# Performance work log

Hardware: AMD Instinct MI355X
Metric: run time of the kernel (lower is better)

Reference implementation:

```python
import jax, jax.numpy as jnp
import numpy as np

N_NODES = 4096
IN_FEATURES = 256
N_HEADS = 8
N_HIDDEN = 32  # out_features // n_heads = 256 // 8
NEG_SLOPE = 0.2
MASK_FILL = -1e9


def setup_inputs() -> dict:
    key = jax.random.key(0)
    k_h, k_adj, k_w, k_a = jax.random.split(key, 4)
    h = jax.random.normal(k_h, (N_NODES, IN_FEATURES), dtype=jnp.float32)
    adj_mat = jax.random.randint(k_adj, (N_NODES, N_NODES, 1), 0, 2, dtype=jnp.int32)
    # linear: Linear(in_features, n_hidden*n_heads, bias=False) -> W: [in, H*F]
    W = jax.random.normal(k_w, (IN_FEATURES, N_HEADS * N_HIDDEN), dtype=jnp.float32) / np.sqrt(IN_FEATURES)
    # attn: Linear(2*n_hidden, 1, bias=False) -> a: [2*F]
    a = jax.random.normal(k_a, (2 * N_HIDDEN,), dtype=jnp.float32) / np.sqrt(2 * N_HIDDEN)
    return {"h": h, "adj_mat": adj_mat, "W": W, "a": a}


def reference(h, adj_mat, W, a):
    n = h.shape[0]
    # g: [n, H, F]
    g = (h @ W).reshape(n, N_HEADS, N_HIDDEN)
    # attn(concat(g_i, g_j)) == g_i . a[:F] + g_j . a[F:]  (decomposed, same math,
    # avoids materializing the O(N^2 * H * 2F) concat tensor of the torch code)
    a_src, a_dst = a[:N_HIDDEN], a[N_HIDDEN:]
    s_src = jnp.einsum('nhf,f->nh', g, a_src)  # [n, H]
    s_dst = jnp.einsum('nhf,f->nh', g, a_dst)  # [n, H]
    e = jax.nn.leaky_relu(s_src[:, None, :] + s_dst[None, :, :], negative_slope=NEG_SLOPE)  # [n, n, H]
    e = jnp.where(adj_mat == 0, MASK_FILL, e)  # adj_mat [n, n, 1] broadcasts over heads
    att = jax.nn.softmax(e, axis=1)  # softmax over source nodes j (dropout in eval mode = identity)
    out = jnp.einsum('ijh,jhf->ihf', att, g)  # [n, H, F]
    return out.reshape(n, N_HEADS * N_HIDDEN)  # is_concat=True
```

## Files before the change

### kernel.cpp

```cpp
#include <hip/hip_runtime.h>

#define NN 4096
#define FIN 256
#define CC 256
#define NH 8
#define NW32 (NN / 32)

typedef __attribute__((ext_vector_type(8))) short short8;
typedef __attribute__((ext_vector_type(4))) float f32x4;
typedef __attribute__((ext_vector_type(4))) unsigned int u32x4;

__device__ __forceinline__ unsigned cvtpk_bf16(float lo, float hi) {
  unsigned r;
  asm("v_cvt_pk_bf16_f32 %0, %1, %2" : "=v"(r) : "v"(lo), "v"(hi));
  return r;
}

__device__ __forceinline__ unsigned short bf16rn(float x) {
  unsigned int u = __builtin_bit_cast(unsigned int, x);
  u += 0x7fffu + ((u >> 16) & 1u);
  return (unsigned short)(u >> 16);
}

__device__ __forceinline__ void gl_lds16(const void* g, void* l) {
  __builtin_amdgcn_global_load_lds(
      (const __attribute__((address_space(1))) void*)g,
      (__attribute__((address_space(3))) void*)l, 16, 0, 0);
}

#define GROWS 8
__global__ __launch_bounds__(256) void k_gemm(
    const float* __restrict__ h, const float* __restrict__ W,
    const float* __restrict__ a, const int* __restrict__ adj,
    unsigned int* __restrict__ adjb, unsigned short* __restrict__ gTs,
    float4* __restrict__ spack, float* __restrict__ dtc) {
  __shared__ float hs[GROWS][FIN];
  const int t = threadIdx.x;

  {
    const int rbase = blockIdx.x * 8;
#pragma unroll
    for (int k = 0; k < 4; ++k) {
      const int idx = k * 256 + t;
      const int r = idx >> 7, wd = idx & 127;
      const int* src = adj + (size_t)(rbase + r) * NN + wd * 32;
      unsigned int bits = 0;
#pragma unroll
      for (int s = 0; s < 8; ++s) {
        const int4 v = *(const int4*)&src[s * 4];
        bits |= (v.x ? 1u : 0u) << (s * 4 + 0);
        bits |= (v.y ? 1u : 0u) << (s * 4 + 1);
        bits |= (v.z ? 1u : 0u) << (s * 4 + 2);
        bits |= (v.w ? 1u : 0u) << (s * 4 + 3);
      }
      adjb[(size_t)(rbase + r) * NW32 + wd] = bits;
    }
  }

  const int r0 = blockIdx.x * GROWS;
#pragma unroll
  for (int idx = t; idx < GROWS * FIN / 4; idx += 256) {
    const int r = idx >> 6, c4 = idx & 63;
    *(float4*)&hs[r][c4 * 4] =
        *(const float4*)&h[(size_t)(r0 + r) * FIN + c4 * 4];
  }
  __syncthreads();
  const int c = t;
  float acc[GROWS];
#pragma unroll
  for (int r = 0; r < GROWS; ++r) acc[r] = 0.f;
  for (int k = 0; k < FIN; k += 4) {
    const float w0 = W[(size_t)(k + 0) * CC + c];
    const float w1 = W[(size_t)(k + 1) * CC + c];
    const float w2 = W[(size_t)(k + 2) * CC + c];
    const float w3 = W[(size_t)(k + 3) * CC + c];
#pragma unroll
    for (int r = 0; r < GROWS; ++r) {
      const float4 hv = *(const float4*)&hs[r][k];
      acc[r] += hv.x * w0 + hv.y * w1 + hv.z * w2 + hv.w * w3;
    }
  }
  const int f = c & 31, hh = c >> 5;
  const float aS = a[f], aD = a[32 + f];
  unsigned short gu[GROWS];
#pragma unroll
  for (int r = 0; r < GROWS; ++r) {
    float ps = acc[r] * aS, pd = acc[r] * aD;
#pragma unroll
    for (int m = 1; m < 32; m <<= 1) {
      ps += __shfl_xor(ps, m, 64);
      pd += __shfl_xor(pd, m, 64);
    }
    if (f == 0) {
      const int n = r0 + r;
      spack[(size_t)hh * NN + n] =
          make_float4(ps, __expf(ps), __expf(0.2f * ps), 0.f);
      float* dc = dtc + (size_t)(n >> 5) * 768 + hh * 32 + (n & 31);
      dc[0] = -pd;
      dc[256] = __expf(pd);
      dc[512] = __expf(0.2f * pd);
    }
    gu[r] = bf16rn(acc[r]);
  }
  uint4 gv;
  gv.x = (unsigned)gu[0] | ((unsigned)gu[1] << 16);
  gv.y = (unsigned)gu[2] | ((unsigned)gu[3] << 16);
  gv.z = (unsigned)gu[4] | ((unsigned)gu[5] << 16);
  gv.w = (unsigned)gu[6] | ((unsigned)gu[7] << 16);
  const int jc = r0 >> 5, qq = (r0 >> 3) & 3;
  const int p = qq ^ ((c >> 1) & 3);
  *(uint4*)(gTs + ((size_t)jc * 1024 + c * 4 + p) * 8) = gv;
}

struct Buf {
  unsigned short gt[8192];
  float dt[3][NH][32];
};

__global__ __launch_bounds__(256, 2) void k_attn(
    const unsigned int* __restrict__ adjb, const unsigned short* __restrict__ gTs,
    const float4* __restrict__ spack, const float* __restrict__ dtc,
    float* __restrict__ acc_ws, float* __restrict__ l_ws,
    float* __restrict__ out, const int splits, const int direct) {
  __shared__ Buf buf[2];

  const int lane = threadIdx.x & 63;
  const int w = threadIdx.x >> 6;
  const int il = lane & 15, q = lane >> 4;
  const int bx = blockIdx.x;
  const int sp = bx & (splits - 1);
  const int ib = bx / splits;
  const int i0w = ib * 64 + (w >> 1) * 32;
  const int hquad = w & 1;
  const int jrange = NN / splits, j0b = sp * jrange;
  const int c0 = (j0b >> 5);

  float ssv[4][2], e1v[4][2], e2v[4][2];
#pragma unroll
  for (int hp = 0; hp < 4; ++hp)
#pragma unroll
    for (int it = 0; it < 2; ++it) {
      const float4 v =
          spack[(size_t)(hquad * 4 + hp) * NN + i0w + it * 16 + il];
      ssv[hp][it] = v.x; e1v[hp][it] = v.y; e2v[hp][it] = v.z;
    }

  f32x4 acc[4][2][2];
  f32x4 lac[4][2];
#pragma unroll
  for (int hp = 0; hp < 4; ++hp)
#pragma unroll
    for (int it = 0; it < 2; ++it) {
#pragma unroll
      for (int r = 0; r < 4; ++r) lac[hp][it][r] = 0.f;
#pragma unroll
      for (int ft = 0; ft < 2; ++ft)
#pragma unroll
        for (int r = 0; r < 4; ++r) acc[hp][it][ft][r] = 0.f;
    }

  const short8 ones = {(short)0x3F80, (short)0x3F80, (short)0x3F80,
                       (short)0x3F80, (short)0x3F80, (short)0x3F80,
                       (short)0x3F80, (short)0x3F80};

  const unsigned int* ab0 = adjb + (size_t)(i0w + il) * NW32 + (j0b >> 5);
  const unsigned int* ab1 = adjb + (size_t)(i0w + 16 + il) * NW32 + (j0b >> 5);
  const int sh = q * 8;
  const int sswz = (il >> 1) & 3;
  const int pswz = q ^ sswz;

  auto stage = [&](Buf* b, int jc) {
    const unsigned short* src = gTs + (size_t)(c0 + jc) * 8192;
#pragma unroll
    for (int pass = 0; pass < 4; ++pass) {
      const int base = pass * 256 + w * 64;
      gl_lds16(src + (size_t)(base + lane) * 8, (char*)b->gt + base * 16);
    }
    if (w < 3) {
      const float* dsrc = dtc + (size_t)(c0 + jc) * 768;
      gl_lds16(dsrc + (size_t)(w * 64 + lane) * 4,
               (char*)&b->dt[0][0][0] + (w * 64) * 16);
    }
  };

  const int nch = jrange / 32;
  stage(&buf[0], 0);
  unsigned int pb0 = ab0[0], pb1 = ab1[0];
  __syncthreads();
  int cur = 0;

  for (int jc = 0; jc < nch; ++jc) {
    if (jc + 1 < nch) stage(&buf[cur ^ 1], jc + 1);
    const Buf* bc = &buf[cur];

    float adf[2][8];
    {
      const unsigned int bits0 = pb0, bits1 = pb1;
#pragma unroll
      for (int e = 0; e < 8; ++e) {
        adf[0][e] = (float)((bits0 >> (sh + e)) & 1u);
        adf[1][e] = (float)((bits1 >> (sh + e)) & 1u);
      }
      if (jc + 1 < nch) { pb0 = ab0[jc + 1]; pb1 = ab1[jc + 1]; }
    }

#pragma unroll
    for (int hp = 0; hp < 4; ++hp) {
      const int hh = hquad * 4 + hp;
      float nsd[8], e1j[8], e2j[8];
      *(float4*)&nsd[0] = *(const float4*)&bc->dt[0][hh][q * 8];
      *(float4*)&nsd[4] = *(const float4*)&bc->dt[0][hh][q * 8 + 4];
      *(float4*)&e1j[0] = *(const float4*)&bc->dt[1][hh][q * 8];
      *(float4*)&e1j[4] = *(const float4*)&bc->dt[1][hh][q * 8 + 4];
      *(float4*)&e2j[0] = *(const float4*)&bc->dt[2][hh][q * 8];
      *(float4*)&e2j[4] = *(const float4*)&bc->dt[2][hh][q * 8 + 4];
      const int u0 = (hh * 32 + il) * 4 + pswz;
      const short8 b0 = *(const short8*)&bc->gt[u0 * 8];
      const short8 b1 = *(const short8*)&bc->gt[(u0 + 64) * 8];
#pragma unroll
      for (int it = 0; it < 2; ++it) {
        const float ssl = ssv[hp][it];
        const float ei1 = e1v[hp][it], ei2 = e2v[hp][it];
        float wv[8];
#pragma unroll
        for (int e = 0; e < 8; ++e) {
          const bool pos = ssl > nsd[e];
          wv[e] = (pos ? ei1 : ei2) * (pos ? e1j[e] : e2j[e]) * adf[it][e];
        }
        u32x4 uu;
#pragma unroll
        for (int m = 0; m < 4; ++m)
          uu[m] = cvtpk_bf16(wv[2 * m], wv[2 * m + 1]);
        const short8 afr = __builtin_bit_cast(short8, uu);
        acc[hp][it][0] = __builtin_amdgcn_mfma_f32_16x16x32_bf16(
            afr, b0, acc[hp][it][0], 0, 0, 0);
        acc[hp][it][1] = __builtin_amdgcn_mfma_f32_16x16x32_bf16(
            afr, b1, acc[hp][it][1], 0, 0, 0);
        lac[hp][it] = __builtin_amdgcn_mfma_f32_16x16x32_bf16(
            afr, ones, lac[hp][it], 0, 0, 0);
      }
    }
    __syncthreads();
    cur ^= 1;
  }

  if (direct) {
#pragma unroll
    for (int hp = 0; hp < 4; ++hp) {
      const int hh = hquad * 4 + hp;
#pragma unroll
      for (int it = 0; it < 2; ++it)
#pragma unroll
        for (int r = 0; r < 4; ++r) {
          const float inv = 1.f / lac[hp][it][r];
          const size_t irow = i0w + it * 16 + q * 4 + r;
#pragma unroll
          for (int ft = 0; ft < 2; ++ft)
            out[irow * CC + hh * 32 + ft * 16 + il] =
                acc[hp][it][ft][r] * inv;
        }
    }
  } else {
#pragma unroll
    for (int hp = 0; hp < 4; ++hp) {
      const int hh = hquad * 4 + hp;
#pragma unroll
      for (int it = 0; it < 2; ++it)
#pragma unroll
        for (int r = 0; r < 4; ++r) {
          const size_t irow = i0w + it * 16 + q * 4 + r;
          if (il == 0)
            l_ws[((size_t)sp * NH + hh) * NN + irow] = lac[hp][it][r];
#pragma unroll
          for (int ft = 0; ft < 2; ++ft)
            acc_ws[((size_t)sp * NN + irow) * CC + hh * 32 + ft * 16 + il] =
                acc[hp][it][ft][r];
        }
    }
  }
}

__global__ __launch_bounds__(256) void k_combine(
    const float* __restrict__ acc_ws, const float* __restrict__ l_ws,
    float* __restrict__ out, const int splits) {
  const int idx = blockIdx.x * 256 + threadIdx.x;
  const int row = idx >> 6, c4 = idx & 63;
  const int hh = c4 >> 3;
  float ax = 0.f, ay = 0.f, az = 0.f, aw = 0.f, l = 0.f;
  for (int s = 0; s < splits; ++s) {
    const float4 v =
        *(const float4*)&acc_ws[((size_t)s * NN + row) * CC + c4 * 4];
    ax += v.x; ay += v.y; az += v.z; aw += v.w;
    l += l_ws[((size_t)s * NH + hh) * NN + row];
  }
  const float inv = 1.f / l;
  *(float4*)&out[(size_t)row * CC + c4 * 4] =
      make_float4(ax * inv, ay * inv, az * inv, aw * inv);
}

extern "C" void kernel_launch(void* const* d_in, const int* in_sizes, int n_in,
                              void* d_out, int out_size, void* d_ws,
                              size_t ws_size, hipStream_t stream) {
  (void)in_sizes; (void)n_in; (void)out_size;
  const float* h = (const float*)d_in[0];
  const int* adj = (const int*)d_in[1];
  const float* W = (const float*)d_in[2];
  const float* a = (const float*)d_in[3];
  float* out = (float*)d_out;
  char* ws = (char*)d_ws;

  unsigned short* gTs = (unsigned short*)ws;
  float4* spack = (float4*)(ws + (size_t)NN * CC * 2);
  float* dtc = (float*)(spack + (size_t)NH * NN);
  unsigned int* adjb =
      (unsigned int*)(dtc + (size_t)(NN / 32) * 768);
  char* after = (char*)(adjb + (size_t)NN * NW32);
  const size_t base = (size_t)(after - ws);
  const size_t per_split = (size_t)NN * CC * 4 + (size_t)NH * NN * 4;

  int splits = 1;
  if (ws_size >= base + 8 * per_split) splits = 8;
  else if (ws_size >= base + 4 * per_split) splits = 4;
  else if (ws_size >= base + 2 * per_split) splits = 2;

  k_gemm<<<NN / GROWS, 256, 0, stream>>>(h, W, a, adj, adjb, gTs, spack, dtc);

  const int nblk = (NN / 64) * splits;
  if (splits == 1) {
    k_attn<<<nblk, 256, 0, stream>>>(adjb, gTs, spack, dtc, nullptr, nullptr,
                                     out, 1, 1);
  } else {
    float* acc_ws = (float*)after;
    float* l_ws = acc_ws + (size_t)splits * NN * CC;
    k_attn<<<nblk, 256, 0, stream>>>(adjb, gTs, spack, dtc, acc_ws, l_ws, out,
                                     splits, 0);
    k_combine<<<NN * CC / 4 / 256, 256, 0, stream>>>(acc_ws, l_ws, out,
                                                     splits);
  }
}
```

Measured before the change: 80.66 us.

## Use max-of-exponentials for leaky-relu weights, ballot-pack adjacency, smaller attn tiles

The attention weight exp(leakyrelu(s_i+s_j)) is now computed as max(e^{s_i}e^{s_j}, e^{0.2s_i}e^{0.2s_j}). Because exp is monotonic, this equals the old sign-branch select and removes the stored score and its comparison from the staged per-source data. Adjacency bit-packing switches from per-thread int4 loads to coalesced per-lane loads combined with wave ballots writing 64-bit words. The attention kernel splits work into 32-row blocks with each wave handling 2 heads instead of 4, which doubles the grid and raises the launch-bounds occupancy target. The trade-off is less reuse of the staged g and adjacency data per block, plus possible subtle overflow or rounding differences in the product form.

```diff
diff --git a/kernel.cpp b/kernel.cpp
--- a/kernel.cpp
+++ b/kernel.cpp
@@ -36,24 +36,21 @@
     float4* __restrict__ spack, float* __restrict__ dtc) {
   __shared__ float hs[GROWS][FIN];
   const int t = threadIdx.x;
+  const int lane = t & 63, w = t >> 6;
 
   {
     const int rbase = blockIdx.x * 8;
 #pragma unroll
-    for (int k = 0; k < 4; ++k) {
-      const int idx = k * 256 + t;
-      const int r = idx >> 7, wd = idx & 127;
-      const int* src = adj + (size_t)(rbase + r) * NN + wd * 32;
-      unsigned int bits = 0;
-#pragma unroll
-      for (int s = 0; s < 8; ++s) {
-        const int4 v = *(const int4*)&src[s * 4];
-        bits |= (v.x ? 1u : 0u) << (s * 4 + 0);
-        bits |= (v.y ? 1u : 0u) << (s * 4 + 1);
-        bits |= (v.z ? 1u : 0u) << (s * 4 + 2);
-        bits |= (v.w ? 1u : 0u) << (s * 4 + 3);
+    for (int r = 0; r < 2; ++r) {
+      const int row = rbase + w * 2 + r;
+      const int* src = adj + (size_t)row * NN;
+      unsigned long long* dst = (unsigned long long*)(adjb + (size_t)row * NW32);
+#pragma unroll 4
+      for (int g = 0; g < 64; ++g) {
+        const int v = src[g * 64 + lane];
+        const unsigned long long b = __ballot(v != 0);
+        if (lane == 0) dst[g] = b;
       }
-      adjb[(size_t)(rbase + r) * NW32 + wd] = bits;
     }
   }
 
@@ -94,11 +91,10 @@
     if (f == 0) {
       const int n = r0 + r;
       spack[(size_t)hh * NN + n] =
-          make_float4(ps, __expf(ps), __expf(0.2f * ps), 0.f);
-      float* dc = dtc + (size_t)(n >> 5) * 768 + hh * 32 + (n & 31);
-      dc[0] = -pd;
-      dc[256] = __expf(pd);
-      dc[512] = __expf(0.2f * pd);
+          make_float4(__expf(ps), __expf(0.2f * ps), 0.f, 0.f);
+      float* dc = dtc + (size_t)(n >> 5) * 512 + hh * 32 + (n & 31);
+      dc[0] = __expf(pd);
+      dc[256] = __expf(0.2f * pd);
     }
     gu[r] = bf16rn(acc[r]);
   }
@@ -114,10 +110,10 @@
 
 struct Buf {
   unsigned short gt[8192];
-  float dt[3][NH][32];
+  float dt[2][NH][32];
 };
 
-__global__ __launch_bounds__(256, 2) void k_attn(
+__global__ __launch_bounds__(256, 4) void k_attn(
     const unsigned int* __restrict__ adjb, const unsigned short* __restrict__ gTs,
     const float4* __restrict__ spack, const float* __restrict__ dtc,
     float* __restrict__ acc_ws, float* __restrict__ l_ws,
@@ -130,25 +126,24 @@
   const int bx = blockIdx.x;
   const int sp = bx & (splits - 1);
   const int ib = bx / splits;
-  const int i0w = ib * 64 + (w >> 1) * 32;
-  const int hquad = w & 1;
+  const int i0 = ib * 32;
+  const int hbase = w * 2;
   const int jrange = NN / splits, j0b = sp * jrange;
-  const int c0 = (j0b >> 5);
-
-  float ssv[4][2], e1v[4][2], e2v[4][2];
-#pragma unroll
-  for (int hp = 0; hp < 4; ++hp)
+  const int c0 = j0b >> 5;
+
+  float e1v[2][2], e2v[2][2];
+#pragma unroll
+  for (int hp = 0; hp < 2; ++hp)
 #pragma unroll
     for (int it = 0; it < 2; ++it) {
-      const float4 v =
-          spack[(size_t)(hquad * 4 + hp) * NN + i0w + it * 16 + il];
-      ssv[hp][it] = v.x; e1v[hp][it] = v.y; e2v[hp][it] = v.z;
-    }
-
-  f32x4 acc[4][2][2];
-  f32x4 lac[4][2];
-#pragma unroll
-  for (int hp = 0; hp < 4; ++hp)
+      const float4 v = spack[(size_t)(hbase + hp) * NN + i0 + it * 16 + il];
+      e1v[hp][it] = v.x; e2v[hp][it] = v.y;
+    }
+
+  f32x4 acc[2][2][2];
+  f32x4 lac[2][2];
+#pragma unroll
+  for (int hp = 0; hp < 2; ++hp)
 #pragma unroll
     for (int it = 0; it < 2; ++it) {
 #pragma unroll
@@ -163,11 +158,10 @@
                        (short)0x3F80, (short)0x3F80, (short)0x3F80,
                        (short)0x3F80, (short)0x3F80};
 
-  const unsigned int* ab0 = adjb + (size_t)(i0w + il) * NW32 + (j0b >> 5);
-  const unsigned int* ab1 = adjb + (size_t)(i0w + 16 + il) * NW32 + (j0b >> 5);
+  const unsigned int* ab0 = adjb + (size_t)(i0 + il) * NW32 + (j0b >> 5);
+  const unsigned int* ab1 = adjb + (size_t)(i0 + 16 + il) * NW32 + (j0b >> 5);
   const int sh = q * 8;
-  const int sswz = (il >> 1) & 3;
-  const int pswz = q ^ sswz;
+  const int pswz = q ^ ((il >> 1) & 3);
 
   auto stage = [&](Buf* b, int jc) {
     const unsigned short* src = gTs + (size_t)(c0 + jc) * 8192;
@@ -176,8 +170,8 @@
       const int base = pass * 256 + w * 64;
       gl_lds16(src + (size_t)(base + lane) * 8, (char*)b->gt + base * 16);
     }
-    if (w < 3) {
-      const float* dsrc = dtc + (size_t)(c0 + jc) * 768;
+    if (w < 2) {
+      const float* dsrc = dtc + (size_t)(c0 + jc) * 512;
       gl_lds16(dsrc + (size_t)(w * 64 + lane) * 4,
                (char*)&b->dt[0][0][0] + (w * 64) * 16);
     }
@@ -205,28 +199,23 @@
     }
 
 #pragma unroll
-    for (int hp = 0; hp < 4; ++hp) {
-      const int hh = hquad * 4 + hp;
-      float nsd[8], e1j[8], e2j[8];
-      *(float4*)&nsd[0] = *(const float4*)&bc->dt[0][hh][q * 8];
-      *(float4*)&nsd[4] = *(const float4*)&bc->dt[0][hh][q * 8 + 4];
-      *(float4*)&e1j[0] = *(const float4*)&bc->dt[1][hh][q * 8];
-      *(float4*)&e1j[4] = *(const float4*)&bc->dt[1][hh][q * 8 + 4];
-      *(float4*)&e2j[0] = *(const float4*)&bc->dt[2][hh][q * 8];
-      *(float4*)&e2j[4] = *(const float4*)&bc->dt[2][hh][q * 8 + 4];
+    for (int hp = 0; hp < 2; ++hp) {
+      const int hh = hbase + hp;
+      float e1j[8], e2j[8];
+      *(float4*)&e1j[0] = *(const float4*)&bc->dt[0][hh][q * 8];
+      *(float4*)&e1j[4] = *(const float4*)&bc->dt[0][hh][q * 8 + 4];
+      *(float4*)&e2j[0] = *(const float4*)&bc->dt[1][hh][q * 8];
+      *(float4*)&e2j[4] = *(const float4*)&bc->dt[1][hh][q * 8 + 4];
       const int u0 = (hh * 32 + il) * 4 + pswz;
       const short8 b0 = *(const short8*)&bc->gt[u0 * 8];
       const short8 b1 = *(const short8*)&bc->gt[(u0 + 64) * 8];
 #pragma unroll
       for (int it = 0; it < 2; ++it) {
-        const float ssl = ssv[hp][it];
         const float ei1 = e1v[hp][it], ei2 = e2v[hp][it];
         float wv[8];
 #pragma unroll
-        for (int e = 0; e < 8; ++e) {
-          const bool pos = ssl > nsd[e];
-          wv[e] = (pos ? ei1 : ei2) * (pos ? e1j[e] : e2j[e]) * adf[it][e];
-        }
+        for (int e = 0; e < 8; ++e)
+          wv[e] = fmaxf(ei1 * e1j[e], ei2 * e2j[e]) * adf[it][e];
         u32x4 uu;
 #pragma unroll
         for (int m = 0; m < 4; ++m)
@@ -246,14 +235,14 @@
 
   if (direct) {
 #pragma unroll
-    for (int hp = 0; hp < 4; ++hp) {
-      const int hh = hquad * 4 + hp;
+    for (int hp = 0; hp < 2; ++hp) {
+      const int hh = hbase + hp;
 #pragma unroll
       for (int it = 0; it < 2; ++it)
 #pragma unroll
         for (int r = 0; r < 4; ++r) {
           const float inv = 1.f / lac[hp][it][r];
-          const size_t irow = i0w + it * 16 + q * 4 + r;
+          const size_t irow = i0 + it * 16 + q * 4 + r;
 #pragma unroll
           for (int ft = 0; ft < 2; ++ft)
             out[irow * CC + hh * 32 + ft * 16 + il] =
@@ -262,13 +251,13 @@
     }
   } else {
 #pragma unroll
-    for (int hp = 0; hp < 4; ++hp) {
-      const int hh = hquad * 4 + hp;
+    for (int hp = 0; hp < 2; ++hp) {
+      const int hh = hbase + hp;
 #pragma unroll
       for (int it = 0; it < 2; ++it)
 #pragma unroll
         for (int r = 0; r < 4; ++r) {
-          const size_t irow = i0w + it * 16 + q * 4 + r;
+          const size_t irow = i0 + it * 16 + q * 4 + r;
           if (il == 0)
             l_ws[((size_t)sp * NH + hh) * NN + irow] = lac[hp][it][r];
 #pragma unroll
@@ -313,7 +302,7 @@
   float4* spack = (float4*)(ws + (size_t)NN * CC * 2);
   float* dtc = (float*)(spack + (size_t)NH * NN);
   unsigned int* adjb =
-      (unsigned int*)(dtc + (size_t)(NN / 32) * 768);
+      (unsigned int*)(dtc + (size_t)(NN / 32) * 512);
   char* after = (char*)(adjb + (size_t)NN * NW32);
   const size_t base = (size_t)(after - ws);
   const size_t per_split = (size_t)NN * CC * 4 + (size_t)NH * NN * 4;
@@ -325,7 +314,7 @@
 
   k_gemm<<<NN / GROWS, 256, 0, stream>>>(h, W, a, adj, adjb, gTs, spack, dtc);
 
-  const int nblk = (NN / 64) * splits;
+  const int nblk = (NN / 32) * splits;
   if (splits == 1) {
     k_attn<<<nblk, 256, 0, stream>>>(adjb, gTs, spack, dtc, nullptr, nullptr,
                                      out, 1, 1);
```

Result: slower. 112.8 us (+39.8%).
